# Kernel optimization log

Hardware: AMD Instinct MI355X
Metric: run time of the kernel (lower is better)

## Reference

```python
import jax, jax.numpy as jnp
import numpy as np

GAMMA = 2.0       # focal gamma (alpha=4.0 is unused in the original forward)
NC_LOOP = 20      # original loops cls in range(n_classes + 1) = 20 classes


def setup_inputs() -> dict:
    key = jax.random.key(0)
    k1, k2 = jax.random.split(key)
    B, C, H, W = 8, 20, 512, 512
    predictions = jax.random.normal(k1, (B, C, H, W), dtype=jnp.float32)
    labels = jax.random.randint(k2, (B, H, W), 0, C)
    # one-hot float target mask [B, C, H, W], as expected by BCE + argmax(dim=1)
    targets = jax.nn.one_hot(labels, C, axis=1, dtype=jnp.float32)
    return {"predictions": predictions, "targets": targets}


def reference(predictions, targets):
    p = jax.nn.softmax(predictions, axis=1)          # [B,C,H,W]
    bs = p.shape[0]
    ps = p.reshape(bs, -1)
    ts = targets.reshape(bs, -1)

    # BCELoss(reduction='none').mean(1); torch clamps log at -100
    log_p = jnp.clip(jnp.log(ps), -100.0)
    log_1mp = jnp.clip(jnp.log1p(-ps), -100.0)
    lseg = (-(ts * log_p + (1.0 - ts) * log_1mp)).mean(axis=1)  # [B]

    # focal loss: sum over class dim, mean over spatial dims
    fl = (-(targets * jnp.log(p + 1e-9)) * (1.0 - p) ** GAMMA).sum(axis=1)  # [B,H,W]
    fcl = fl.mean(axis=(1, 2))  # [B]

    # per-class IoU via per-batch class histograms (fused confusion-count pass)
    preds = jnp.argmax(p, axis=1).reshape(bs, -1)        # [B, HW]
    tgt = jnp.argmax(targets, axis=1).reshape(bs, -1)    # [B, HW]
    cnt_tgt = jax.vmap(lambda t: jnp.bincount(t, length=NC_LOOP))(tgt)     # [B,NC]
    cnt_pred = jax.vmap(lambda t: jnp.bincount(t, length=NC_LOOP))(preds)  # [B,NC]
    match = (preds == tgt).astype(jnp.float32)
    tp = jax.vmap(lambda t, w: jnp.bincount(t, weights=w, length=NC_LOOP))(tgt, match)
    fp = cnt_pred.astype(jnp.float32) - tp
    fn = cnt_tgt.astype(jnp.float32) - tp
    denom = tp + fp + fn
    # torch.nan_to_num(TP/denom): 0/0 -> 0
    iou_c = jnp.where(denom > 0, tp / jnp.maximum(denom, 1.0), 0.0)
    ious = iou_c.sum(axis=1)                                # [B]
    present = (cnt_tgt > 0).astype(jnp.float32).sum(axis=1)  # [B]
    iou = ious / present
    liou = 1.0 - iou

    return (lseg + liou + fcl).mean()
```

## Files before the change

kernel.cpp:

```cpp
#include <hip/hip_runtime.h>

#define NCLS 20
#define HW   (512 * 512)
#define TPB  256
#define PPT  4

#define ACC_STRIDE 64

typedef float v4f __attribute__((ext_vector_type(4)));

__global__ __launch_bounds__(256) void seg_label(
    const float* __restrict__ tgt, unsigned char* __restrict__ lab,
    unsigned nf4)
{
    const unsigned NTHR = 4096u * 256u;
    for (unsigned e4 = blockIdx.x * 256u + threadIdx.x; e4 < nf4; e4 += NTHR) {
        const v4f v = __builtin_nontemporal_load(
            reinterpret_cast<const v4f*>(tgt) + e4);
        const unsigned f   = e4 * 4u;
        const unsigned c   = (f >> 18) % NCLS;
        const unsigned bb  = f / (NCLS * HW);
        const unsigned pix = f & (HW - 1);
        unsigned char* lp = lab + (size_t)bb * HW + pix;
        if (v.x > 0.5f) lp[0] = (unsigned char)c;
        if (v.y > 0.5f) lp[1] = (unsigned char)c;
        if (v.z > 0.5f) lp[2] = (unsigned char)c;
        if (v.w > 0.5f) lp[3] = (unsigned char)c;
    }
}

__global__ __launch_bounds__(TPB, 5) void seg_main(
    const float* __restrict__ pred,
    const unsigned char* __restrict__ lab,
    unsigned* __restrict__ acc)
{
    __shared__ unsigned h_tgt[NCLS], h_pred[NCLS], h_tp[NCLS];
    __shared__ float red[8];

    const int tid = threadIdx.x;
    if (tid < NCLS) { h_tgt[tid] = 0u; h_pred[tid] = 0u; h_tp[tid] = 0u; }
    __syncthreads();

    const int b = blockIdx.y;
    const size_t pix = ((size_t)blockIdx.x * TPB + tid) * PPT;

    const unsigned voff = (unsigned)(pix * 4u);
    const unsigned long long pbase =
        (unsigned long long)(uintptr_t)pred + (unsigned long long)b * (NCLS * HW * 4ull);
#define SB(c) const unsigned long long sb##c = pbase + (unsigned long long)(c) * (HW * 4ull);
    SB(0) SB(1) SB(2) SB(3) SB(4) SB(5) SB(6) SB(7) SB(8) SB(9)
    SB(10) SB(11) SB(12) SB(13) SB(14) SB(15) SB(16) SB(17) SB(18) SB(19)
    const unsigned long long sbl =
        (unsigned long long)(uintptr_t)lab + (unsigned long long)b * HW;
    const unsigned voffl = (unsigned)pix;

#define DECLPX(P) \
    float M1_##P = 0.0f, M2_##P = 0.0f, M3_##P = 0.0f, M4_##P = 0.0f, \
          M5_##P = 0.0f, mx_##P = -1e30f, xl_##P = 0.0f; \
    int pa_##P = 0;
    DECLPX(0) DECLPX(1) DECLPX(2) DECLPX(3)

    v4f xv0, xv1, xv2, xv3, xv4, xv5, xv6, xv7, xv8, xv9,
        xv10, xv11, xv12, xv13, xv14, xv15, xv16, xv17, xv18, xv19;
    unsigned labu;

#define ISSUE4(c0, c1, c2, c3)                                              \
    asm volatile(                                                           \
        "global_load_dwordx4 %0, %4, %5\n\t"                                \
        "global_load_dwordx4 %1, %4, %6\n\t"                                \
        "global_load_dwordx4 %2, %4, %7\n\t"                                \
        "global_load_dwordx4 %3, %4, %8"                                    \
        : "=&v"(xv##c0), "=&v"(xv##c1), "=&v"(xv##c2), "=&v"(xv##c3)        \
        : "v"(voff), "s"(sb##c0), "s"(sb##c1), "s"(sb##c2), "s"(sb##c3))

#define WAITV(N)                                              \
    asm volatile("s_waitcnt vmcnt(" #N ")" ::: "memory");     \
    __builtin_amdgcn_sched_barrier(0)

#define PROC1(c, X, P) {                                                    \
    const float x_ = (X);                                                   \
    const float e_ = __expf(x_);                                            \
    const float e2_ = e_ * e_, e3_ = e2_ * e_, e4_ = e2_ * e2_,             \
                e5_ = e3_ * e2_;                                            \
    M1_##P += e_; M2_##P += e2_; M3_##P += e3_; M4_##P += e4_;              \
    M5_##P += e5_;                                                          \
    const bool b_ = x_ > mx_##P;                                            \
    mx_##P = b_ ? x_ : mx_##P;  pa_##P = b_ ? (c) : pa_##P;                 \
    xl_##P = ((c) == lb##P) ? x_ : xl_##P; }

#define PROCC(c) PROC1(c, xv##c.x, 0) PROC1(c, xv##c.y, 1) \
                 PROC1(c, xv##c.z, 2) PROC1(c, xv##c.w, 3)
#define PROC4(c0, c1, c2, c3) PROCC(c0) PROCC(c1) PROCC(c2) PROCC(c3)

    asm volatile("global_load_dword %0, %1, %2"
                 : "=&v"(labu) : "v"(voffl), "s"(sbl));
    ISSUE4(0, 1, 2, 3);
    ISSUE4(4, 5, 6, 7);
    ISSUE4(8, 9, 10, 11);
    WAITV(12);
    const int lb0 = (int)(labu & 0xffu);
    const int lb1 = (int)((labu >> 8) & 0xffu);
    const int lb2 = (int)((labu >> 16) & 0xffu);
    const int lb3 = (int)(labu >> 24);
    WAITV(8);   PROC4(0, 1, 2, 3);   ISSUE4(12, 13, 14, 15);
    WAITV(8);   PROC4(4, 5, 6, 7);   ISSUE4(16, 17, 18, 19);
    WAITV(8);   PROC4(8, 9, 10, 11);
    WAITV(4);   PROC4(12, 13, 14, 15);
    WAITV(0);   PROC4(16, 17, 18, 19);

    float tl = 0.0f, tf = 0.0f;
#define FINPX(P) {                                                          \
    const float S_ = M1_##P;                                                \
    const float is_ = 1.0f / S_;                                            \
    const float is2_ = is_ * is_;                                           \
    const float logS_ = __logf(S_);                                         \
    const float ser_ = 1.0f + 0.5f * M2_##P * is2_                          \
                     + 0.33333333f * M3_##P * is2_ * is_                    \
                     + 0.25f * M4_##P * is2_ * is2_                         \
                     + 0.2f * M5_##P * is2_ * is2_ * is_;                   \
    const float loglab_ = xl_##P - logS_;                                   \
    const float plab_ = __expf(xl_##P) * is_;                               \
    const float l1m_ = __logf(fmaxf(1.0f - plab_, 1e-37f));                 \
    tl += ser_ + l1m_ - loglab_;                                            \
    const float om_ = 1.0f - plab_;                                         \
    tf -= loglab_ * om_ * om_;                                              \
    atomicAdd(&h_tgt[lb##P], 1u);                                           \
    atomicAdd(&h_pred[pa_##P], 1u);                                         \
    if (pa_##P == lb##P) atomicAdd(&h_tp[lb##P], 1u); }

    FINPX(0) FINPX(1) FINPX(2) FINPX(3)

#pragma unroll
    for (int off = 32; off > 0; off >>= 1) {
        tl += __shfl_down(tl, off, 64);
        tf += __shfl_down(tf, off, 64);
    }
    const int wid = tid >> 6, lane = tid & 63;
    if (lane == 0) { red[wid] = tl; red[4 + wid] = tf; }
    __syncthreads();

    unsigned* ab = acc + (size_t)b * ACC_STRIDE;
    if (tid == 0) {
        const float a = red[0] + red[1] + red[2] + red[3];
        const float f = red[4] + red[5] + red[6] + red[7];
        atomicAdd(reinterpret_cast<float*>(ab + 0), a);
        atomicAdd(reinterpret_cast<float*>(ab + 1), f);
    }
    if (tid < NCLS) {
        atomicAdd(&ab[2  + tid], h_tgt[tid]);
        atomicAdd(&ab[22 + tid], h_pred[tid]);
        atomicAdd(&ab[42 + tid], h_tp[tid]);
    }
}

__global__ __launch_bounds__(256) void seg_final(
    const unsigned* __restrict__ acc, float* __restrict__ out, int nb)
{
    __shared__ float bl[8];
    const int tid = threadIdx.x;
    const int b = tid >> 5, c = tid & 31;

    float iou_c = 0.0f, pres = 0.0f;
    if (b < nb && c < NCLS) {
        const unsigned* ab = acc + (size_t)b * ACC_STRIDE;
        unsigned tg = ab[2 + c], pd = ab[22 + c], tpv = ab[42 + c];
        unsigned denom = tg + pd - tpv;
        if (tg > 0) pres = 1.0f;
        if (denom > 0) iou_c = (float)tpv / (float)denom;
    }
#pragma unroll
    for (int off = 16; off > 0; off >>= 1) {
        iou_c += __shfl_down(iou_c, off, 32);
        pres  += __shfl_down(pres,  off, 32);
    }
    if (c == 0 && b < nb) {
        const unsigned* ab = acc + (size_t)b * ACC_STRIDE;
        const float*    fs = reinterpret_cast<const float*>(ab);
        float lseg = fs[0] * (1.0f / ((float)NCLS * (float)HW));
        float fcl  = fs[1] * (1.0f / (float)HW);
        float iou  = (pres > 0.0f) ? (iou_c / pres) : 0.0f;
        bl[b] = lseg + (1.0f - iou) + fcl;
    }
    __syncthreads();
    if (tid == 0) {
        float t = 0.0f;
        for (int i = 0; i < nb; ++i) t += bl[i];
        out[0] = t / (float)nb;
    }
}

extern "C" void kernel_launch(void* const* d_in, const int* in_sizes, int n_in,
                              void* d_out, int out_size, void* d_ws, size_t ws_size,
                              hipStream_t stream)
{
    const float* pred = (const float*)d_in[0];
    const float* tgt  = (const float*)d_in[1];
    float* out = (float*)d_out;
    unsigned* acc = (unsigned*)d_ws;
    unsigned char* labels = (unsigned char*)d_ws + 4096;

    const int nb = in_sizes[0] / (NCLS * HW);
    const unsigned nf4 = (unsigned)(in_sizes[1] / 4);

    (void)hipMemsetAsync(acc, 0, (size_t)nb * ACC_STRIDE * sizeof(unsigned), stream);

    seg_label<<<4096, 256, 0, stream>>>(tgt, labels, nf4);

    dim3 grid(HW / (TPB * PPT), nb);
    seg_main<<<grid, TPB, 0, stream>>>(pred, labels, acc);
    seg_final<<<1, 256, 0, stream>>>(acc, out, nb);
}
```

Baseline: 83.62 us.

## Fold memset and final reduction into kernels, truncate log series with argmax correction

The accumulator memset now happens inside the label kernel. The final IoU/loss reduction now runs in the last block of the main kernel, found through an atomic completion counter, so two launches are gone. The per-class power series for the BCE log(1-p) term is cut from five moments to three. An exact correction term is added for the argmax class, whose probability can be large, which removes per-element multiplies and accumulators. This relies on the other classes having small probabilities for the truncated series to stay accurate, and it adds a threadfence plus a global atomic at the end of every block.

```diff
diff --git a/kernel.cpp b/kernel.cpp
--- a/kernel.cpp
+++ b/kernel.cpp
@@ -11,8 +11,11 @@
 
 __global__ __launch_bounds__(256) void seg_label(
     const float* __restrict__ tgt, unsigned char* __restrict__ lab,
-    unsigned nf4)
+    unsigned* __restrict__ acc, unsigned accw, unsigned nf4)
 {
+    if (blockIdx.x == 0) {
+        for (unsigned i = threadIdx.x; i <= accw; i += 256u) acc[i] = 0u;
+    }
     const unsigned NTHR = 4096u * 256u;
     for (unsigned e4 = blockIdx.x * 256u + threadIdx.x; e4 < nf4; e4 += NTHR) {
         const v4f v = __builtin_nontemporal_load(
@@ -32,10 +35,12 @@
 __global__ __launch_bounds__(TPB, 5) void seg_main(
     const float* __restrict__ pred,
     const unsigned char* __restrict__ lab,
-    unsigned* __restrict__ acc)
+    unsigned* __restrict__ acc,
+    float* __restrict__ out, int nb)
 {
     __shared__ unsigned h_tgt[NCLS], h_pred[NCLS], h_tp[NCLS];
     __shared__ float red[8];
+    __shared__ unsigned isLast;
 
     const int tid = threadIdx.x;
     if (tid < NCLS) { h_tgt[tid] = 0u; h_pred[tid] = 0u; h_tp[tid] = 0u; }
@@ -55,8 +60,8 @@
     const unsigned voffl = (unsigned)pix;
 
 #define DECLPX(P) \
-    float M1_##P = 0.0f, M2_##P = 0.0f, M3_##P = 0.0f, M4_##P = 0.0f, \
-          M5_##P = 0.0f, mx_##P = -1e30f, xl_##P = 0.0f; \
+    float M1_##P = 0.0f, M2_##P = 0.0f, M3_##P = 0.0f, \
+          mx_##P = -1e30f, xl_##P = 0.0f; \
     int pa_##P = 0;
     DECLPX(0) DECLPX(1) DECLPX(2) DECLPX(3)
 
@@ -80,10 +85,10 @@
 #define PROC1(c, X, P) {                                                    \
     const float x_ = (X);                                                   \
     const float e_ = __expf(x_);                                            \
-    const float e2_ = e_ * e_, e3_ = e2_ * e_, e4_ = e2_ * e2_,             \
-                e5_ = e3_ * e2_;                                            \
-    M1_##P += e_; M2_##P += e2_; M3_##P += e3_; M4_##P += e4_;              \
-    M5_##P += e5_;                                                          \
+    const float e2_ = e_ * e_;                                              \
+    M1_##P += e_;                                                           \
+    M2_##P += e2_;                                                          \
+    M3_##P = __builtin_fmaf(e2_, e_, M3_##P);                               \
     const bool b_ = x_ > mx_##P;                                            \
     mx_##P = b_ ? x_ : mx_##P;  pa_##P = b_ ? (c) : pa_##P;                 \
     xl_##P = ((c) == lb##P) ? x_ : xl_##P; }
@@ -110,18 +115,18 @@
 
     float tl = 0.0f, tf = 0.0f;
 #define FINPX(P) {                                                          \
-    const float S_ = M1_##P;                                                \
-    const float is_ = 1.0f / S_;                                            \
-    const float is2_ = is_ * is_;                                           \
+    const float S_ = M1_##P, is_ = 1.0f / S_, is2_ = is_ * is_;             \
     const float logS_ = __logf(S_);                                         \
-    const float ser_ = 1.0f + 0.5f * M2_##P * is2_                          \
-                     + 0.33333333f * M3_##P * is2_ * is_                    \
-                     + 0.25f * M4_##P * is2_ * is2_                         \
-                     + 0.2f * M5_##P * is2_ * is2_ * is_;                   \
+    const float T3_ = 1.0f + 0.5f * M2_##P * is2_                           \
+                    + 0.33333333f * M3_##P * is2_ * is_;                    \
+    const float ppa_ = __expf(mx_##P) * is_;                                \
+    const float Rpa_ = -__logf(fmaxf(1.0f - ppa_, 1e-12f)) - ppa_           \
+                     - 0.5f * ppa_ * ppa_                                   \
+                     - 0.33333333f * ppa_ * ppa_ * ppa_;                    \
     const float loglab_ = xl_##P - logS_;                                   \
     const float plab_ = __expf(xl_##P) * is_;                               \
     const float l1m_ = __logf(fmaxf(1.0f - plab_, 1e-37f));                 \
-    tl += ser_ + l1m_ - loglab_;                                            \
+    tl += T3_ + Rpa_ + l1m_ - loglab_;                                      \
     const float om_ = 1.0f - plab_;                                         \
     tf -= loglab_ * om_ * om_;                                              \
     atomicAdd(&h_tgt[lb##P], 1u);                                           \
@@ -151,41 +156,46 @@
         atomicAdd(&ab[22 + tid], h_pred[tid]);
         atomicAdd(&ab[42 + tid], h_tp[tid]);
     }
-}
-
-__global__ __launch_bounds__(256) void seg_final(
-    const unsigned* __restrict__ acc, float* __restrict__ out, int nb)
-{
-    __shared__ float bl[8];
-    const int tid = threadIdx.x;
-    const int b = tid >> 5, c = tid & 31;
-
-    float iou_c = 0.0f, pres = 0.0f;
-    if (b < nb && c < NCLS) {
-        const unsigned* ab = acc + (size_t)b * ACC_STRIDE;
-        unsigned tg = ab[2 + c], pd = ab[22 + c], tpv = ab[42 + c];
-        unsigned denom = tg + pd - tpv;
-        if (tg > 0) pres = 1.0f;
-        if (denom > 0) iou_c = (float)tpv / (float)denom;
-    }
+
+    __syncthreads();
+    if (tid == 0) {
+        __threadfence();
+        const unsigned done = atomicAdd(&acc[(size_t)nb * ACC_STRIDE], 1u);
+        isLast = (done == gridDim.x * gridDim.y - 1u) ? 1u : 0u;
+    }
+    __syncthreads();
+    if (isLast) {
+        const int fb = tid >> 5, fc = tid & 31;
+        float iou_c = 0.0f, pres = 0.0f;
+        if (fb < nb && fc < NCLS) {
+            unsigned* fab = acc + (size_t)fb * ACC_STRIDE;
+            unsigned tg  = atomicOr(&fab[2  + fc], 0u);
+            unsigned pd  = atomicOr(&fab[22 + fc], 0u);
+            unsigned tpv = atomicOr(&fab[42 + fc], 0u);
+            unsigned denom = tg + pd - tpv;
+            if (tg > 0) pres = 1.0f;
+            if (denom > 0) iou_c = (float)tpv / (float)denom;
+        }
 #pragma unroll
-    for (int off = 16; off > 0; off >>= 1) {
-        iou_c += __shfl_down(iou_c, off, 32);
-        pres  += __shfl_down(pres,  off, 32);
-    }
-    if (c == 0 && b < nb) {
-        const unsigned* ab = acc + (size_t)b * ACC_STRIDE;
-        const float*    fs = reinterpret_cast<const float*>(ab);
-        float lseg = fs[0] * (1.0f / ((float)NCLS * (float)HW));
-        float fcl  = fs[1] * (1.0f / (float)HW);
-        float iou  = (pres > 0.0f) ? (iou_c / pres) : 0.0f;
-        bl[b] = lseg + (1.0f - iou) + fcl;
-    }
-    __syncthreads();
-    if (tid == 0) {
-        float t = 0.0f;
-        for (int i = 0; i < nb; ++i) t += bl[i];
-        out[0] = t / (float)nb;
+        for (int off = 16; off > 0; off >>= 1) {
+            iou_c += __shfl_down(iou_c, off, 32);
+            pres  += __shfl_down(pres,  off, 32);
+        }
+        if (fc == 0 && fb < nb) {
+            unsigned* fab = acc + (size_t)fb * ACC_STRIDE;
+            float s0 = atomicAdd(reinterpret_cast<float*>(fab + 0), 0.0f);
+            float s1 = atomicAdd(reinterpret_cast<float*>(fab + 1), 0.0f);
+            float lseg = s0 * (1.0f / ((float)NCLS * (float)HW));
+            float fcl  = s1 * (1.0f / (float)HW);
+            float iou  = (pres > 0.0f) ? (iou_c / pres) : 0.0f;
+            red[fb] = lseg + (1.0f - iou) + fcl;
+        }
+        __syncthreads();
+        if (tid == 0) {
+            float t = 0.0f;
+            for (int i = 0; i < nb; ++i) t += red[i];
+            out[0] = t / (float)nb;
+        }
     }
 }
 
@@ -202,11 +212,9 @@
     const int nb = in_sizes[0] / (NCLS * HW);
     const unsigned nf4 = (unsigned)(in_sizes[1] / 4);
 
-    (void)hipMemsetAsync(acc, 0, (size_t)nb * ACC_STRIDE * sizeof(unsigned), stream);
-
-    seg_label<<<4096, 256, 0, stream>>>(tgt, labels, nf4);
+    seg_label<<<4096, 256, 0, stream>>>(tgt, labels, acc,
+                                        (unsigned)(nb * ACC_STRIDE), nf4);
 
     dim3 grid(HW / (TPB * PPT), nb);
-    seg_main<<<grid, TPB, 0, stream>>>(pred, labels, acc);
-    seg_final<<<1, 256, 0, stream>>>(acc, out, nb);
+    seg_main<<<grid, TPB, 0, stream>>>(pred, labels, acc, out, nb);
 }
```

Measured after the change: 130.8 us. 56.4% more time.
